# Performance work log

Measured on AMD Instinct MI355X. Metric: run time of the kernel, lower is better.

Reference implementation:

```python
import jax, jax.numpy as jnp
import numpy as np

N_ENT, N_REL, D, E, NS, B = 100000, 200, 64, 1000000, 4096, 32


def setup_inputs() -> dict:
    key = jax.random.key(0)
    ks = jax.random.split(key, 20)
    s = 1.0 / np.sqrt(D)
    # rotational relation embeddings: [cos|sin ; cos|-sin] -> [2*N_REL, D]
    phases = (2 * np.pi * np.random.RandomState(0).rand(N_REL, D // 2)).astype(np.float32)
    rel = np.concatenate([
        np.concatenate([np.cos(phases), np.sin(phases)], -1),
        np.concatenate([np.cos(phases), -np.sin(phases)], -1)], 0)
    inp = {
        'ent_emb': jax.random.normal(ks[0], (N_ENT, D), jnp.float32) * s,
        'rel_emb': jnp.asarray(rel),
        'gcn_W': jax.random.normal(ks[1], (2, D, D), jnp.float32) * s,
        'gcn_b': jnp.zeros((2, D), jnp.float32),
        'mm_W0': jax.random.normal(ks[2], (3 * D, D), jnp.float32) * s,
        'mm_b0': jnp.zeros((D,), jnp.float32),
        'mm_W1': jax.random.normal(ks[3], (D, D), jnp.float32) * s,
        'mm_b1': jnp.zeros((D,), jnp.float32),
        'mm_Wadv': jax.random.normal(ks[4], (D, 3), jnp.float32) * s,
        'mm_badv': jnp.zeros((3,), jnp.float32),
        'mm_Wval': jax.random.normal(ks[5], (D, 1), jnp.float32) * s,
        'mm_bval': jnp.zeros((1,), jnp.float32),
        'ex_W0': jax.random.normal(ks[6], (D, D), jnp.float32) * s,
        'ex_b0': jnp.zeros((D,), jnp.float32),
        'ex_W1': jax.random.normal(ks[7], (D, D), jnp.float32) * s,
        'ex_b1': jnp.zeros((D,), jnp.float32),
        'ex_Wadv': jax.random.normal(ks[8], (D, 5), jnp.float32) * s,
        'ex_badv': jnp.zeros((5,), jnp.float32),
        'ex_Wval': jax.random.normal(ks[9], (D, 1), jnp.float32) * s,
        'ex_bval': jnp.zeros((1,), jnp.float32),
        'edge_index': jax.random.randint(ks[10], (2, E), 0, N_ENT, jnp.int32),
        'edge_type': jax.random.randint(ks[11], (E,), 0, 2 * N_REL, jnp.int32),
        'short_idx': jax.random.randint(ks[12], (NS,), 0, E, jnp.int32),
        'agent_idx': jax.random.randint(ks[13], (B,), 0, N_ENT, jnp.int32),
    }
    return inp


def _dueling_mlp(h, W0, b0, W1, b1, Wadv, badv, Wval, bval):
    h = jax.nn.relu(h @ W0 + b0)
    h = jax.nn.relu(h @ W1 + b1)
    adv = h @ Wadv + badv
    val = h @ Wval + bval
    return val + adv - adv.mean(-1, keepdims=True)


def reference(ent_emb, rel_emb, gcn_W, gcn_b, mm_W0, mm_b0, mm_W1, mm_b1,
              mm_Wadv, mm_badv, mm_Wval, mm_bval, ex_W0, ex_b0, ex_W1, ex_b1,
              ex_Wadv, ex_badv, ex_Wval, ex_bval,
              edge_index, edge_type, short_idx, agent_idx):
    n = ent_emb.shape[0]
    src, dst = edge_index[0], edge_index[1]
    x = ent_emb
    for l in range(gcn_W.shape[0]):  # GCNConv, normalize=False, no self-loops
        msg = (x @ gcn_W[l])[src]                      # [E, D] gather-transform
        x = jax.ops.segment_sum(msg, dst, num_segments=n) + gcn_b[l]
        x = jax.nn.relu(x)                             # dropout is identity in eval
    # memory-management head: concat(head, relation, tail) for short-term triples
    h_mm = jnp.concatenate([x[src[short_idx]], rel_emb[edge_type[short_idx]],
                            x[dst[short_idx]]], axis=-1)  # [NS, 3D]
    q_mm = _dueling_mlp(h_mm, mm_W0, mm_b0, mm_W1, mm_b1, mm_Wadv, mm_badv, mm_Wval, mm_bval)
    # explore head: agent-node embedding
    q_ex = _dueling_mlp(x[agent_idx], ex_W0, ex_b0, ex_W1, ex_b1, ex_Wadv, ex_badv, ex_Wval, ex_bval)
    return q_mm, q_ex
```

## Files before the change

kernel.cpp:

```cpp
#include <hip/hip_runtime.h>

#define DD 64
#define CAP 32

typedef short bf16x8 __attribute__((ext_vector_type(8)));
typedef float f32x4 __attribute__((ext_vector_type(4)));

static __device__ __forceinline__ unsigned short f2bf(float f) {
  unsigned u = __float_as_uint(f);
  return (unsigned short)((u + 0x7fffu + ((u >> 16) & 1u)) >> 16);
}
static __device__ __forceinline__ unsigned pack2bf(float lo, float hi) {
  return (((unsigned)f2bf(hi)) << 16) | (unsigned)f2bf(lo);
}


__global__ __launch_bounds__(256) void k_zero(
    int* __restrict__ f4, int nf4, int* __restrict__ cnt, int N) {
  const int i = blockIdx.x * 256 + threadIdx.x;
  if (i < nf4) f4[i] = 0;
  if (i < N) cnt[i] = 0;
}

__global__ __launch_bounds__(256) void k_flag2(
    const int* __restrict__ sidx, const int* __restrict__ src,
    const int* __restrict__ dst, const int* __restrict__ aidx,
    unsigned char* __restrict__ flags, int NS, int B) {
  const int i = blockIdx.x * 256 + threadIdx.x;
  if (i < NS) {
    int e = sidx[i];
    flags[src[e]] = 1;
    flags[dst[e]] = 1;
  } else if (i < NS + B) {
    flags[aidx[i - NS]] = 1;
  }
}

__device__ __forceinline__ void gemm_body(
    const float* __restrict__ x, const float* __restrict__ W,
    unsigned short* __restrict__ yh, int N, int bid, int nB) {
  __shared__ unsigned short wt[DD * DD];
  __shared__ float ys[4][16][68];
  for (int i = threadIdx.x; i < DD * DD; i += 256) {
    int k = i >> 6, n = i & 63;
    wt[n * DD + k] = f2bf(W[i]);
  }
  __syncthreads();
  const int wave = threadIdx.x >> 6;
  const int lane = threadIdx.x & 63;
  const int g = lane >> 4;
  const int m = lane & 15;
  bf16x8 bfr[8];
#pragma unroll
  for (int nt = 0; nt < 4; ++nt)
#pragma unroll
    for (int m2 = 0; m2 < 2; ++m2) {
      const int base = (nt * 16 + m) * DD + 4 * g + 32 * m2;
      ushort4 lo = *(const ushort4*)&wt[base];
      ushort4 hi = *(const ushort4*)&wt[base + 16];
      bf16x8 f;
      f[0] = (short)lo.x; f[1] = (short)lo.y; f[2] = (short)lo.z; f[3] = (short)lo.w;
      f[4] = (short)hi.x; f[5] = (short)hi.y; f[6] = (short)hi.z; f[7] = (short)hi.w;
      bfr[nt * 2 + m2] = f;
    }
  const int tiles = (N + 15) / 16;
  for (int t = bid * 4 + wave; t < tiles; t += nB * 4) {
    const int row = t * 16 + m;
    const int rsafe = (row < N) ? row : (N - 1);
    const float* xr = x + (size_t)rsafe * DD + 4 * g;
    float4 a0 = *(const float4*)(xr + 0);
    float4 a1 = *(const float4*)(xr + 16);
    float4 a2 = *(const float4*)(xr + 32);
    float4 a3 = *(const float4*)(xr + 48);
    bf16x8 af0, af1;
    af0[0] = (short)f2bf(a0.x); af0[1] = (short)f2bf(a0.y);
    af0[2] = (short)f2bf(a0.z); af0[3] = (short)f2bf(a0.w);
    af0[4] = (short)f2bf(a1.x); af0[5] = (short)f2bf(a1.y);
    af0[6] = (short)f2bf(a1.z); af0[7] = (short)f2bf(a1.w);
    af1[0] = (short)f2bf(a2.x); af1[1] = (short)f2bf(a2.y);
    af1[2] = (short)f2bf(a2.z); af1[3] = (short)f2bf(a2.w);
    af1[4] = (short)f2bf(a3.x); af1[5] = (short)f2bf(a3.y);
    af1[6] = (short)f2bf(a3.z); af1[7] = (short)f2bf(a3.w);
    f32x4 acc0 = {0.f, 0.f, 0.f, 0.f}, acc1 = acc0, acc2 = acc0, acc3 = acc0;
    acc0 = __builtin_amdgcn_mfma_f32_16x16x32_bf16(af0, bfr[0], acc0, 0, 0, 0);
    acc0 = __builtin_amdgcn_mfma_f32_16x16x32_bf16(af1, bfr[1], acc0, 0, 0, 0);
    acc1 = __builtin_amdgcn_mfma_f32_16x16x32_bf16(af0, bfr[2], acc1, 0, 0, 0);
    acc1 = __builtin_amdgcn_mfma_f32_16x16x32_bf16(af1, bfr[3], acc1, 0, 0, 0);
    acc2 = __builtin_amdgcn_mfma_f32_16x16x32_bf16(af0, bfr[4], acc2, 0, 0, 0);
    acc2 = __builtin_amdgcn_mfma_f32_16x16x32_bf16(af1, bfr[5], acc2, 0, 0, 0);
    acc3 = __builtin_amdgcn_mfma_f32_16x16x32_bf16(af0, bfr[6], acc3, 0, 0, 0);
    acc3 = __builtin_amdgcn_mfma_f32_16x16x32_bf16(af1, bfr[7], acc3, 0, 0, 0);
#pragma unroll
    for (int r = 0; r < 4; ++r) {
      ys[wave][4 * g + r][0 * 16 + m] = acc0[r];
      ys[wave][4 * g + r][1 * 16 + m] = acc1[r];
      ys[wave][4 * g + r][2 * 16 + m] = acc2[r];
      ys[wave][4 * g + r][3 * 16 + m] = acc3[r];
    }
    if (row < N) {
      unsigned short* yr = yh + (size_t)row * DD + g * 16;
      const float* s = &ys[wave][m][g * 16];
      uint4 olo, ohi;
      olo.x = pack2bf(s[0], s[1]);
      olo.y = pack2bf(s[2], s[3]);
      olo.z = pack2bf(s[4], s[5]);
      olo.w = pack2bf(s[6], s[7]);
      ohi.x = pack2bf(s[8], s[9]);
      ohi.y = pack2bf(s[10], s[11]);
      ohi.z = pack2bf(s[12], s[13]);
      ohi.w = pack2bf(s[14], s[15]);
      *(uint4*)yr = olo;
      *(uint4*)(yr + 8) = ohi;
    }
  }
}

__global__ __launch_bounds__(256) void k_pre2(
    const float* __restrict__ x, const float* __restrict__ W,
    unsigned short* __restrict__ yh, int N, int GB,
    const int* __restrict__ src, const int* __restrict__ dst,
    unsigned char* __restrict__ flags, int* __restrict__ cnt,
    int* __restrict__ csr, int E) {
  const int bid = blockIdx.x;
  if (bid < GB) {
    gemm_body(x, W, yh, N, bid, GB);
  } else {
    int e = (bid - GB) * 256 + threadIdx.x;
    if (e < E) {
      int d = dst[e];
      int s = src[e];
      int slot = atomicAdd(&cnt[d], 1);
      if (slot < CAP) csr[d * CAP + slot] = s;
      if (flags[d] & 1) flags[s] = flags[s] | 2;
    }
  }
}

__global__ __launch_bounds__(256) void k_gemm(
    const float* __restrict__ x, const float* __restrict__ W,
    unsigned short* __restrict__ yh, int N) {
  gemm_body(x, W, yh, N, blockIdx.x, gridDim.x);
}

__global__ __launch_bounds__(256) void k_gather_h(
    const unsigned short* __restrict__ yh, const int* __restrict__ cnt,
    const int* __restrict__ csr, const float* __restrict__ b,
    float* __restrict__ outp, int N, const unsigned char* __restrict__ flags,
    int bit) {
  const int wave = threadIdx.x >> 6;
  const int lane = threadIdx.x & 63;
  const int h = lane >> 5;
  const int c = lane & 31;
  const int n = blockIdx.x * 4 + wave;
  if (n >= N) return;
  if (!(flags[n] & bit)) return;
  const float b0r = b[2 * c];
  const float b1r = b[2 * c + 1];
  int i = n * CAP;
  int c2 = cnt[n];
  c2 = (c2 < CAP) ? c2 : CAP;
  const int end = i + c2;
  float a0 = 0.f, a1 = 0.f;
  for (; i + 8 <= end; i += 8) {
    int ib = __builtin_amdgcn_readfirstlane(i);
    int sA = csr[ib + 0 + h];
    int sB = csr[ib + 2 + h];
    int sC = csr[ib + 4 + h];
    int sD = csr[ib + 6 + h];
    unsigned vA = *(const unsigned*)&yh[(size_t)sA * DD + 2 * c];
    unsigned vB = *(const unsigned*)&yh[(size_t)sB * DD + 2 * c];
    unsigned vC = *(const unsigned*)&yh[(size_t)sC * DD + 2 * c];
    unsigned vD = *(const unsigned*)&yh[(size_t)sD * DD + 2 * c];
    a0 += (__uint_as_float(vA << 16) + __uint_as_float(vB << 16)) +
          (__uint_as_float(vC << 16) + __uint_as_float(vD << 16));
    a1 += (__uint_as_float(vA & 0xffff0000u) + __uint_as_float(vB & 0xffff0000u)) +
          (__uint_as_float(vC & 0xffff0000u) + __uint_as_float(vD & 0xffff0000u));
  }
  for (; i + 2 <= end; i += 2) {
    int sA = csr[__builtin_amdgcn_readfirstlane(i) + h];
    unsigned vA = *(const unsigned*)&yh[(size_t)sA * DD + 2 * c];
    a0 += __uint_as_float(vA << 16);
    a1 += __uint_as_float(vA & 0xffff0000u);
  }
  if (i < end && h == 0) {
    int sA = csr[i];
    unsigned vA = *(const unsigned*)&yh[(size_t)sA * DD + 2 * c];
    a0 += __uint_as_float(vA << 16);
    a1 += __uint_as_float(vA & 0xffff0000u);
  }
  a0 += __shfl_xor(a0, 32);
  a1 += __shfl_xor(a1, 32);
  if (h == 0) {
    float2 r;
    r.x = fmaxf(a0 + b0r, 0.f);
    r.y = fmaxf(a1 + b1r, 0.f);
    *(float2*)&outp[(size_t)n * DD + 2 * c] = r;
  }
}

__global__ __launch_bounds__(256) void k_transform(
    const float* __restrict__ x, const float* __restrict__ W,
    float* __restrict__ y, int n_rows, int relu_in) {
  __shared__ __align__(16) float Ws[DD * DD];
  __shared__ __align__(16) float xs[4][DD];
  for (int i = threadIdx.x; i < DD * DD; i += 256) Ws[i] = W[i];
  __syncthreads();
  const int wave = threadIdx.x >> 6;
  const int lane = threadIdx.x & 63;
  for (int n = blockIdx.x * 4 + wave; n < n_rows; n += gridDim.x * 4) {
    float xv = x[n * DD + lane];
    if (relu_in) xv = fmaxf(xv, 0.f);
    xs[wave][lane] = xv;
    float acc = 0.f;
#pragma unroll
    for (int k4 = 0; k4 < DD / 4; ++k4) {
      float4 h4 = *(const float4*)&xs[wave][k4 * 4];
      acc = fmaf(h4.x, Ws[(k4 * 4 + 0) * DD + lane], acc);
      acc = fmaf(h4.y, Ws[(k4 * 4 + 1) * DD + lane], acc);
      acc = fmaf(h4.z, Ws[(k4 * 4 + 2) * DD + lane], acc);
      acc = fmaf(h4.w, Ws[(k4 * 4 + 3) * DD + lane], acc);
    }
    y[n * DD + lane] = acc;
  }
}

__global__ __launch_bounds__(256) void k_init_bias(
    float4* __restrict__ acc, const float* __restrict__ b, int total4) {
  const float4* b4 = (const float4*)b;
  for (int i = blockIdx.x * blockDim.x + threadIdx.x; i < total4;
       i += gridDim.x * blockDim.x)
    acc[i] = b4[i & 15];
}

__global__ __launch_bounds__(256) void k_scatter(
    const float* __restrict__ y, const int* __restrict__ src,
    const int* __restrict__ dst, float* __restrict__ acc, int E) {
  const int total = E * 16;
  for (int i = blockIdx.x * blockDim.x + threadIdx.x; i < total;
       i += gridDim.x * blockDim.x) {
    int e = i >> 4;
    int d4 = (i & 15) << 2;
    int s = src[e], dd = dst[e];
    float4 v = *(const float4*)&y[s * DD + d4];
    float* ap = &acc[dd * DD + d4];
    unsafeAtomicAdd(ap + 0, v.x);
    unsafeAtomicAdd(ap + 1, v.y);
    unsafeAtomicAdd(ap + 2, v.z);
    unsafeAtomicAdd(ap + 3, v.w);
  }
}

__global__ __launch_bounds__(256) void k_relu_inplace(float* __restrict__ p, int n) {
  for (int i = blockIdx.x * blockDim.x + threadIdx.x; i < n;
       i += gridDim.x * blockDim.x)
    p[i] = fmaxf(p[i], 0.f);
}

__global__ __launch_bounds__(256) void k_heads(
    const float* __restrict__ xact, const float* __restrict__ rel,
    const int* __restrict__ src, const int* __restrict__ dst,
    const int* __restrict__ etype, const int* __restrict__ sidx,
    const float* __restrict__ mmW0, const float* __restrict__ mmB0,
    const float* __restrict__ mmW1, const float* __restrict__ mmB1,
    const float* __restrict__ mmWa, const float* __restrict__ mmBa,
    const float* __restrict__ mmWv, const float* __restrict__ mmBv,
    const float* __restrict__ exW0, const float* __restrict__ exB0,
    const float* __restrict__ exW1, const float* __restrict__ exB1,
    const float* __restrict__ exWa, const float* __restrict__ exBa,
    const float* __restrict__ exWv, const float* __restrict__ exBv,
    const int* __restrict__ aidx, float* __restrict__ q_mm,
    float* __restrict__ q_ex, int NS, int B, int MB) {
  __shared__ __align__(16) float W0s[192 * DD];
  __shared__ float Wadvs[DD * 5], Wvals[DD], b0s[DD], b1s[DD], badvs[5];
  __shared__ __align__(16) float hs[4][192];
  __shared__ __align__(16) float h1s[4][DD];
  const int wave = threadIdx.x >> 6;
  const int lane = threadIdx.x & 63;
  if (blockIdx.x < MB) {
    for (int i = threadIdx.x; i < 192 * DD; i += 256) W0s[i] = mmW0[i];
    for (int i = threadIdx.x; i < DD * 3; i += 256) Wadvs[i] = mmWa[i];
    if (threadIdx.x < DD) {
      Wvals[threadIdx.x] = mmWv[threadIdx.x];
      b0s[threadIdx.x] = mmB0[threadIdx.x];
      b1s[threadIdx.x] = mmB1[threadIdx.x];
    }
    if (threadIdx.x < 3) badvs[threadIdx.x] = mmBa[threadIdx.x];
    __syncthreads();
    const float bv = mmBv[0];
    for (int i = blockIdx.x * 4 + wave; i < NS; i += MB * 4) {
      int e = sidx[i];
      int s = src[e], dd = dst[e], t = etype[e];
      hs[wave][lane] = fmaxf(xact[s * DD + lane], 0.f);
      hs[wave][64 + lane] = rel[t * DD + lane];
      hs[wave][128 + lane] = fmaxf(xact[dd * DD + lane], 0.f);
      float acc = b0s[lane];
#pragma unroll
      for (int k4 = 0; k4 < 48; ++k4) {
        float4 h4 = *(const float4*)&hs[wave][k4 * 4];
        acc = fmaf(h4.x, W0s[(k4 * 4 + 0) * DD + lane], acc);
        acc = fmaf(h4.y, W0s[(k4 * 4 + 1) * DD + lane], acc);
        acc = fmaf(h4.z, W0s[(k4 * 4 + 2) * DD + lane], acc);
        acc = fmaf(h4.w, W0s[(k4 * 4 + 3) * DD + lane], acc);
      }
      h1s[wave][lane] = fmaxf(acc, 0.f);
      float acc2 = b1s[lane];
#pragma unroll
      for (int k4 = 0; k4 < 16; ++k4) {
        float4 h4 = *(const float4*)&h1s[wave][k4 * 4];
        acc2 = fmaf(h4.x, mmW1[(k4 * 4 + 0) * DD + lane], acc2);
        acc2 = fmaf(h4.y, mmW1[(k4 * 4 + 1) * DD + lane], acc2);
        acc2 = fmaf(h4.z, mmW1[(k4 * 4 + 2) * DD + lane], acc2);
        acc2 = fmaf(h4.w, mmW1[(k4 * 4 + 3) * DD + lane], acc2);
      }
      float h2 = fmaxf(acc2, 0.f);
      float p0 = h2 * Wadvs[lane * 3 + 0];
      float p1 = h2 * Wadvs[lane * 3 + 1];
      float p2 = h2 * Wadvs[lane * 3 + 2];
      float pv = h2 * Wvals[lane];
#pragma unroll
      for (int off = 32; off; off >>= 1) {
        p0 += __shfl_xor(p0, off);
        p1 += __shfl_xor(p1, off);
        p2 += __shfl_xor(p2, off);
        pv += __shfl_xor(pv, off);
      }
      if (lane == 0) {
        float a0 = p0 + badvs[0], a1 = p1 + badvs[1], a2 = p2 + badvs[2];
        float val = pv + bv;
        float m = (a0 + a1 + a2) * (1.f / 3.f);
        q_mm[i * 3 + 0] = val + a0 - m;
        q_mm[i * 3 + 1] = val + a1 - m;
        q_mm[i * 3 + 2] = val + a2 - m;
      }
    }
  } else {
    float* W1s = W0s + DD * DD;
    for (int i = threadIdx.x; i < DD * DD; i += 256) {
      W0s[i] = exW0[i];
      W1s[i] = exW1[i];
    }
    for (int i = threadIdx.x; i < DD * 5; i += 256) Wadvs[i] = exWa[i];
    if (threadIdx.x < DD) {
      Wvals[threadIdx.x] = exWv[threadIdx.x];
      b0s[threadIdx.x] = exB0[threadIdx.x];
      b1s[threadIdx.x] = exB1[threadIdx.x];
    }
    if (threadIdx.x < 5) badvs[threadIdx.x] = exBa[threadIdx.x];
    __syncthreads();
    const float bv = exBv[0];
    const int i = (blockIdx.x - MB) * 4 + wave;
    if (i >= B) return;
    int n = aidx[i];
    hs[wave][lane] = fmaxf(xact[n * DD + lane], 0.f);
    float acc = b0s[lane];
#pragma unroll
    for (int k4 = 0; k4 < 16; ++k4) {
      float4 h4 = *(const float4*)&hs[wave][k4 * 4];
      acc = fmaf(h4.x, W0s[(k4 * 4 + 0) * DD + lane], acc);
      acc = fmaf(h4.y, W0s[(k4 * 4 + 1) * DD + lane], acc);
      acc = fmaf(h4.z, W0s[(k4 * 4 + 2) * DD + lane], acc);
      acc = fmaf(h4.w, W0s[(k4 * 4 + 3) * DD + lane], acc);
    }
    h1s[wave][lane] = fmaxf(acc, 0.f);
    float acc2 = b1s[lane];
#pragma unroll
    for (int k4 = 0; k4 < 16; ++k4) {
      float4 h4 = *(const float4*)&h1s[wave][k4 * 4];
      acc2 = fmaf(h4.x, W1s[(k4 * 4 + 0) * DD + lane], acc2);
      acc2 = fmaf(h4.y, W1s[(k4 * 4 + 1) * DD + lane], acc2);
      acc2 = fmaf(h4.z, W1s[(k4 * 4 + 2) * DD + lane], acc2);
      acc2 = fmaf(h4.w, W1s[(k4 * 4 + 3) * DD + lane], acc2);
    }
    float h2 = fmaxf(acc2, 0.f);
    float p[6];
#pragma unroll
    for (int c = 0; c < 5; ++c) p[c] = h2 * Wadvs[lane * 5 + c];
    p[5] = h2 * Wvals[lane];
#pragma unroll
    for (int off = 32; off; off >>= 1)
#pragma unroll
      for (int c = 0; c < 6; ++c) p[c] += __shfl_xor(p[c], off);
    if (lane == 0) {
      float a[5];
      float m = 0.f;
#pragma unroll
      for (int c = 0; c < 5; ++c) {
        a[c] = p[c] + badvs[c];
        m += a[c];
      }
      m *= 0.2f;
      float val = p[5] + bv;
#pragma unroll
      for (int c = 0; c < 5; ++c) q_ex[i * 5 + c] = val + a[c] - m;
    }
  }
}

extern "C" void kernel_launch(void* const* d_in, const int* in_sizes, int n_in,
                              void* d_out, int out_size, void* d_ws, size_t ws_size,
                              hipStream_t stream) {
  const float* ent = (const float*)d_in[0];
  const float* rel = (const float*)d_in[1];
  const float* gcnW = (const float*)d_in[2];
  const float* gcnB = (const float*)d_in[3];
  const float* mmW0 = (const float*)d_in[4];
  const float* mmB0 = (const float*)d_in[5];
  const float* mmW1 = (const float*)d_in[6];
  const float* mmB1 = (const float*)d_in[7];
  const float* mmWa = (const float*)d_in[8];
  const float* mmBa = (const float*)d_in[9];
  const float* mmWv = (const float*)d_in[10];
  const float* mmBv = (const float*)d_in[11];
  const float* exW0 = (const float*)d_in[12];
  const float* exB0 = (const float*)d_in[13];
  const float* exW1 = (const float*)d_in[14];
  const float* exB1 = (const float*)d_in[15];
  const float* exWa = (const float*)d_in[16];
  const float* exBa = (const float*)d_in[17];
  const float* exWv = (const float*)d_in[18];
  const float* exBv = (const float*)d_in[19];
  const int* eidx = (const int*)d_in[20];
  const int* etype = (const int*)d_in[21];
  const int* sidx = (const int*)d_in[22];
  const int* aidx = (const int*)d_in[23];

  const int N = in_sizes[0] / DD;
  const int E = in_sizes[20] / 2;
  const int NS = in_sizes[22];
  const int B = in_sizes[23];
  const int* src = eidx;
  const int* dst = eidx + E;

  float* bufA = (float*)d_ws;
  float* bufB = bufA + (size_t)N * DD;
  int* cnt = (int*)(bufB + (size_t)N * DD);
  unsigned char* flags = (unsigned char*)(cnt + N);
  unsigned short* yh = (unsigned short*)bufA;
  int* csr = (int*)d_ws + (size_t)N * DD / 2;
  const int nf4 = (N + 3) / 4;
  const size_t need = ((size_t)2 * N * DD + (size_t)N) * 4 + (size_t)nf4 * 4;

  float* q_mm = (float*)d_out;
  float* q_ex = q_mm + (size_t)NS * 3;

  dim3 blk(256);
  const int eb = (E + 255) / 256;
  const int GB = 512;
  const int MB = 256;
  const int XB = (B + 3) / 4;

  if (ws_size >= need) {
    k_zero<<<(N + 255) / 256, blk, 0, stream>>>((int*)flags, nf4, cnt, N);
    k_flag2<<<(NS + B + 255) / 256, blk, 0, stream>>>(sidx, src, dst, aidx, flags,
                                                      NS, B);
    k_pre2<<<GB + eb, blk, 0, stream>>>(ent, gcnW, yh, N, GB, src, dst, flags, cnt,
                                        csr, E);
    k_gather_h<<<(N + 3) / 4, blk, 0, stream>>>(yh, cnt, csr, gcnB, bufB, N, flags,
                                                2);
    k_gemm<<<512, blk, 0, stream>>>(bufB, gcnW + DD * DD, yh, N);
    k_gather_h<<<(N + 3) / 4, blk, 0, stream>>>(yh, cnt, csr, gcnB + DD, bufB, N,
                                                flags, 1);
    k_heads<<<MB + XB, blk, 0, stream>>>(bufB, rel, src, dst, etype, sidx, mmW0,
                                         mmB0, mmW1, mmB1, mmWa, mmBa, mmWv, mmBv,
                                         exW0, exB0, exW1, exB1, exWa, exBa, exWv,
                                         exBv, aidx, q_mm, q_ex, NS, B, MB);
  } else {
    k_transform<<<1024, blk, 0, stream>>>(ent, gcnW, bufA, N, 0);
    k_init_bias<<<1024, blk, 0, stream>>>((float4*)bufB, gcnB, N * 16);
    k_scatter<<<2048, blk, 0, stream>>>(bufA, src, dst, bufB, E);
    k_transform<<<1024, blk, 0, stream>>>(bufB, gcnW + DD * DD, bufA, N, 1);
    k_init_bias<<<1024, blk, 0, stream>>>((float4*)bufB, gcnB + DD, N * 16);
    k_scatter<<<2048, blk, 0, stream>>>(bufA, src, dst, bufB, E);
    k_relu_inplace<<<1024, blk, 0, stream>>>(bufB, N * DD);
    k_heads<<<MB + XB, blk, 0, stream>>>(bufB, rel, src, dst, etype, sidx, mmW0,
                                         mmB0, mmW1, mmB1, mmWa, mmBa, mmWv, mmBv,
                                         exW0, exB0, exW1, exB1, exWa, exBa, exWv,
                                         exBv, aidx, q_mm, q_ex, NS, B, MB);
  }
}
```

Baseline: 146.6 us.

## Build CSR only for needed nodes and reorder second GCN layer as aggregate-then-transform

New measurement: 142.5 us. -2.8%, faster.

```diff
diff --git a/kernel.cpp b/kernel.cpp
--- a/kernel.cpp
+++ b/kernel.cpp
@@ -119,27 +119,48 @@
     const float* __restrict__ x, const float* __restrict__ W,
     unsigned short* __restrict__ yh, int N, int GB,
     const int* __restrict__ src, const int* __restrict__ dst,
-    unsigned char* __restrict__ flags, int* __restrict__ cnt,
-    int* __restrict__ csr, int E) {
+    unsigned char* __restrict__ flags, int E) {
   const int bid = blockIdx.x;
   if (bid < GB) {
     gemm_body(x, W, yh, N, bid, GB);
   } else {
+    const int T = (gridDim.x - GB) * 256;
     int e = (bid - GB) * 256 + threadIdx.x;
+#pragma unroll
+    for (int j = 0; j < 4; ++j, e += T) {
+      if (e < E && (flags[dst[e]] & 1)) {
+        int s = src[e];
+        flags[s] = flags[s] | 2;
+      }
+    }
+  }
+}
+
+__global__ __launch_bounds__(256) void k_fillcnt(
+    const int* __restrict__ src, const int* __restrict__ dst,
+    const unsigned char* __restrict__ flags, int* __restrict__ cnt,
+    int* __restrict__ csr, int E) {
+  const int T = gridDim.x * 256;
+  const int e0 = blockIdx.x * 256 + threadIdx.x;
+  int dd[4], ss[4];
+  bool act[4];
+#pragma unroll
+  for (int j = 0; j < 4; ++j) {
+    const int e = e0 + j * T;
+    act[j] = false;
     if (e < E) {
-      int d = dst[e];
-      int s = src[e];
-      int slot = atomicAdd(&cnt[d], 1);
-      if (slot < CAP) csr[d * CAP + slot] = s;
-      if (flags[d] & 1) flags[s] = flags[s] | 2;
-    }
-  }
-}
-
-__global__ __launch_bounds__(256) void k_gemm(
-    const float* __restrict__ x, const float* __restrict__ W,
-    unsigned short* __restrict__ yh, int N) {
-  gemm_body(x, W, yh, N, blockIdx.x, gridDim.x);
+      dd[j] = dst[e];
+      ss[j] = src[e];
+      act[j] = flags[dd[j]] != 0;
+    }
+  }
+#pragma unroll
+  for (int j = 0; j < 4; ++j) {
+    if (act[j]) {
+      int slot = atomicAdd(&cnt[dd[j]], 1);
+      if (slot < CAP) csr[dd[j] * CAP + slot] = ss[j];
+    }
+  }
 }
 
 __global__ __launch_bounds__(256) void k_gather_h(
@@ -198,6 +219,64 @@
   }
 }
 
+__global__ __launch_bounds__(256) void k_gather_s(
+    const float* __restrict__ x1, const int* __restrict__ cnt,
+    const int* __restrict__ csr, unsigned short* __restrict__ s2, int N,
+    const unsigned char* __restrict__ flags) {
+  const int wave = threadIdx.x >> 6;
+  const int lane = threadIdx.x & 63;
+  const int n = blockIdx.x * 4 + wave;
+  if (n >= N) return;
+  if (!(flags[n] & 1)) return;
+  int i = n * CAP;
+  int c2 = cnt[n];
+  c2 = (c2 < CAP) ? c2 : CAP;
+  const int end = i + c2;
+  float a = 0.f;
+  for (; i + 4 <= end; i += 4) {
+    int ib = __builtin_amdgcn_readfirstlane(i);
+    int p0 = csr[ib + 0];
+    int p1 = csr[ib + 1];
+    int p2 = csr[ib + 2];
+    int p3 = csr[ib + 3];
+    a += (x1[(size_t)p0 * DD + lane] + x1[(size_t)p1 * DD + lane]) +
+         (x1[(size_t)p2 * DD + lane] + x1[(size_t)p3 * DD + lane]);
+  }
+  for (; i < end; ++i) {
+    int p = csr[__builtin_amdgcn_readfirstlane(i)];
+    a += x1[(size_t)p * DD + lane];
+  }
+  s2[(size_t)n * DD + lane] = f2bf(a);
+}
+
+__global__ __launch_bounds__(256) void k_xform(
+    const unsigned short* __restrict__ s2, const float* __restrict__ W1,
+    const float* __restrict__ b1, const unsigned char* __restrict__ flags,
+    float* __restrict__ outp, int N) {
+  __shared__ __align__(16) float Ws[DD * DD];
+  __shared__ __align__(16) float xs[4][DD];
+  for (int i = threadIdx.x; i < DD * DD; i += 256) Ws[i] = W1[i];
+  __syncthreads();
+  const int wave = threadIdx.x >> 6;
+  const int lane = threadIdx.x & 63;
+  const float br = b1[lane];
+  for (int n = blockIdx.x * 4 + wave; n < N; n += gridDim.x * 4) {
+    if (!(flags[n] & 1)) continue;
+    unsigned u = s2[(size_t)n * DD + lane];
+    xs[wave][lane] = __uint_as_float(u << 16);
+    float acc = br;
+#pragma unroll
+    for (int k4 = 0; k4 < 16; ++k4) {
+      float4 h4 = *(const float4*)&xs[wave][k4 * 4];
+      acc = fmaf(h4.x, Ws[(k4 * 4 + 0) * DD + lane], acc);
+      acc = fmaf(h4.y, Ws[(k4 * 4 + 1) * DD + lane], acc);
+      acc = fmaf(h4.z, Ws[(k4 * 4 + 2) * DD + lane], acc);
+      acc = fmaf(h4.w, Ws[(k4 * 4 + 3) * DD + lane], acc);
+    }
+    outp[(size_t)n * DD + lane] = fmaxf(acc, 0.f);
+  }
+}
+
 __global__ __launch_bounds__(256) void k_transform(
     const float* __restrict__ x, const float* __restrict__ W,
     float* __restrict__ y, int n_rows, int relu_in) {
@@ -444,8 +523,9 @@
   float* q_ex = q_mm + (size_t)NS * 3;
 
   dim3 blk(256);
-  const int eb = (E + 255) / 256;
   const int GB = 512;
+  const int EB4 = (E + 1023) / 1024;
+  const int FB4 = ((E + 3) / 4 + 255) / 256;
   const int MB = 256;
   const int XB = (B + 3) / 4;
 
@@ -453,24 +533,24 @@
     k_zero<<<(N + 255) / 256, blk, 0, stream>>>((int*)flags, nf4, cnt, N);
     k_flag2<<<(NS + B + 255) / 256, blk, 0, stream>>>(sidx, src, dst, aidx, flags,
                                                       NS, B);
-    k_pre2<<<GB + eb, blk, 0, stream>>>(ent, gcnW, yh, N, GB, src, dst, flags, cnt,
-                                        csr, E);
+    k_pre2<<<GB + EB4, blk, 0, stream>>>(ent, gcnW, yh, N, GB, src, dst, flags, E);
+    k_fillcnt<<<FB4, blk, 0, stream>>>(src, dst, flags, cnt, csr, E);
     k_gather_h<<<(N + 3) / 4, blk, 0, stream>>>(yh, cnt, csr, gcnB, bufB, N, flags,
                                                 2);
-    k_gemm<<<512, blk, 0, stream>>>(bufB, gcnW + DD * DD, yh, N);
-    k_gather_h<<<(N + 3) / 4, blk, 0, stream>>>(yh, cnt, csr, gcnB + DD, bufB, N,
-                                                flags, 1);
+    k_gather_s<<<(N + 3) / 4, blk, 0, stream>>>(bufB, cnt, csr, yh, N, flags);
+    k_xform<<<512, blk, 0, stream>>>(yh, gcnW + DD * DD, gcnB + DD, flags, bufB, N);
     k_heads<<<MB + XB, blk, 0, stream>>>(bufB, rel, src, dst, etype, sidx, mmW0,
                                          mmB0, mmW1, mmB1, mmWa, mmBa, mmWv, mmBv,
                                          exW0, exB0, exW1, exB1, exWa, exBa, exWv,
                                          exBv, aidx, q_mm, q_ex, NS, B, MB);
   } else {
-    k_transform<<<1024, blk, 0, stream>>>(ent, gcnW, bufA, N, 0);
+    float* tmp = bufA;
+    k_transform<<<1024, blk, 0, stream>>>(ent, gcnW, tmp, N, 0);
     k_init_bias<<<1024, blk, 0, stream>>>((float4*)bufB, gcnB, N * 16);
-    k_scatter<<<2048, blk, 0, stream>>>(bufA, src, dst, bufB, E);
-    k_transform<<<1024, blk, 0, stream>>>(bufB, gcnW + DD * DD, bufA, N, 1);
+    k_scatter<<<2048, blk, 0, stream>>>(tmp, src, dst, bufB, E);
+    k_transform<<<1024, blk, 0, stream>>>(bufB, gcnW + DD * DD, tmp, N, 1);
     k_init_bias<<<1024, blk, 0, stream>>>((float4*)bufB, gcnB + DD, N * 16);
-    k_scatter<<<2048, blk, 0, stream>>>(bufA, src, dst, bufB, E);
+    k_scatter<<<2048, blk, 0, stream>>>(tmp, src, dst, bufB, E);
     k_relu_inplace<<<1024, blk, 0, stream>>>(bufB, N * DD);
     k_heads<<<MB + XB, blk, 0, stream>>>(bufB, rel, src, dst, etype, sidx, mmW0,
                                          mmB0, mmW1, mmB1, mmWa, mmBa, mmWv, mmBv,
```
